# Kernel optimization log

Hardware: AMD Instinct MI355X
Metric: run time of the kernel (lower is better)

The kernel has to match this reference:

```python
import jax, jax.numpy as jnp
import numpy as np

BATCH = 32768


def _unpack(packed, n):
    # packed: [rows, ceil(n/8)] ints in [0,256). Extract bits MSB-first per byte.
    bits = (packed[:, :, None] >> jnp.arange(7, -1, -1, dtype=packed.dtype)) & 1
    return bits.reshape(packed.shape[0], -1)[:, :n]  # [rows, n] of {0,1}


def setup_inputs() -> dict:
    key = jax.random.key(0)
    k0, k1, k2, k3, k4 = jax.random.split(key, 5)
    return {
        "x": jax.random.normal(k0, (BATCH, 784), dtype=jnp.float32),
        "w1_packed": jax.random.randint(k1, (256, 98), 0, 256, dtype=jnp.int32),
        "m1_packed": jax.random.randint(k2, (256, 98), 0, 256, dtype=jnp.int32),
        "alpha1": jnp.float32(1.0),
        "w2_packed": jax.random.randint(k3, (10, 32), 0, 256, dtype=jnp.int32),
        "m2_packed": jax.random.randint(k4, (10, 32), 0, 256, dtype=jnp.int32),
        "alpha2": jnp.float32(1.0),
    }


def reference(x, w1_packed, m1_packed, alpha1, w2_packed, m2_packed, alpha2):
    # Layer 1: binary {-1,+1} weights * {0,1} mask * alpha
    w1 = (2 * _unpack(w1_packed, 784) - 1).astype(jnp.float32)
    w1 = w1 * _unpack(m1_packed, 784).astype(jnp.float32) * alpha1  # [256, 784]
    h = jax.nn.relu(jnp.einsum('bi,oi->bo', x, w1))  # [B, 256]
    # Layer 2
    w2 = (2 * _unpack(w2_packed, 256) - 1).astype(jnp.float32)
    w2 = w2 * _unpack(m2_packed, 256).astype(jnp.float32) * alpha2  # [10, 256]
    return jnp.einsum('bh,oh->bo', h, w2)  # [B, 10]
```

## Files before the change

kernel.cpp:

```cpp
#include <hip/hip_runtime.h>
#include <hip/hip_bf16.h>

typedef __bf16 bf16x8 __attribute__((ext_vector_type(8)));
typedef float floatx4 __attribute__((ext_vector_type(4)));

#define GLB_AS __attribute__((address_space(1)))
#define LDS_AS __attribute__((address_space(3)))

__device__ __forceinline__ void async_cp16(const void* g, void* l) {
  __builtin_amdgcn_global_load_lds((GLB_AS void*)g, (LDS_AS void*)l, 16, 0, 0);
}

__device__ __forceinline__ unsigned short f2bf(float f) {
  __bf16 b = (__bf16)f;
  return __builtin_bit_cast(unsigned short, b);
}

__global__ void decode_w1_kernel(const int* __restrict__ w1p,
                                 const int* __restrict__ m1p,
                                 unsigned short* __restrict__ w1d) {
  int t = blockIdx.x * 256 + threadIdx.x;
  if (t >= 256 * 100) return;
  int r = t / 100;
  int j = t - r * 100;
  unsigned short vals[8];
#pragma unroll
  for (int k = 0; k < 8; ++k) vals[k] = 0;
  if (j < 98) {
    unsigned int v = (unsigned int)w1p[r * 98 + j];
    unsigned int m = (unsigned int)m1p[r * 98 + j];
#pragma unroll
    for (int k = 0; k < 8; ++k) {
      unsigned int bit = (v >> (7 - k)) & 1u;
      unsigned int mk  = (m >> (7 - k)) & 1u;
      vals[k] = (unsigned short)(mk ? (bit ? 0x3F80u : 0xBF80u) : 0u);
    }
  }
  uint4 pack;
  pack.x = (unsigned)vals[0] | ((unsigned)vals[1] << 16);
  pack.y = (unsigned)vals[2] | ((unsigned)vals[3] << 16);
  pack.z = (unsigned)vals[4] | ((unsigned)vals[5] << 16);
  pack.w = (unsigned)vals[6] | ((unsigned)vals[7] << 16);
  *reinterpret_cast<uint4*>(w1d + t * 8) = pack;
}

#define BM 64
#define BK 32
#define NCH 25
#define W1LD 800
#define HS_LD 264

#define OFF_WS0 0
#define OFF_WS1 8192
#define OFF_XS0 16384
#define OFF_XS1 18432
#define OFF_HS  0
#define OFF_W2  16896

__global__ __launch_bounds__(256, 2) void fused_kernel(
    const float* __restrict__ x,
    const unsigned short* __restrict__ w1d,
    const int* __restrict__ w2p,
    const int* __restrict__ m2p,
    const float* __restrict__ a1p,
    const float* __restrict__ a2p,
    float* __restrict__ out) {
  __shared__ unsigned short smem[64 * 264 + 16 * 256];

  const int tid  = threadIdx.x;
  const int wave = tid >> 6;
  const int lane = tid & 63;
  const int l15  = lane & 15;
  const int quad = lane >> 4;
  const int row0 = blockIdx.x * BM;

  floatx4 acc[4][4];
#pragma unroll
  for (int i = 0; i < 4; ++i)
#pragma unroll
    for (int j = 0; j < 4; ++j) acc[i][j] = (floatx4){0.f, 0.f, 0.f, 0.f};

  auto stage_w = [&](int kc, int offW) {
#pragma unroll
    for (int it = 0; it < 4; ++it) {
      int seg = it * 256 + tid;
      int r = seg >> 2, c = seg & 3;
      async_cp16(w1d + r * W1LD + kc * BK + c * 8, &smem[offW + seg * 8]);
    }
  };
  auto load_x = [&](int kc, float4* xv) {
#pragma unroll
    for (int it = 0; it < 2; ++it) {
      int seg = it * 256 + tid;
      int r = seg >> 3, c4 = seg & 7;
      int col = kc * BK + c4 * 4;
      if (col < 784) {
        xv[it] = *reinterpret_cast<const float4*>(
            x + (size_t)(row0 + r) * 784 + col);
      } else {
        xv[it] = (float4){0.f, 0.f, 0.f, 0.f};
      }
    }
  };
  auto cvt_write = [&](int offX, const float4* xv) {
#pragma unroll
    for (int it = 0; it < 2; ++it) {
      int seg = it * 256 + tid;
      int r = seg >> 3, c4 = seg & 7;
      ushort4 b;
      b.x = f2bf(xv[it].x); b.y = f2bf(xv[it].y);
      b.z = f2bf(xv[it].z); b.w = f2bf(xv[it].w);
      *reinterpret_cast<ushort4*>(&smem[offX + r * BK + c4 * 4]) = b;
    }
  };
  auto compute = [&](int offW, int offX) {
    bf16x8 af[4], bfr[4];
#pragma unroll
    for (int mi = 0; mi < 4; ++mi)
      af[mi] = *reinterpret_cast<const bf16x8*>(
          &smem[offX + (mi * 16 + l15) * BK + quad * 8]);
#pragma unroll
    for (int nj = 0; nj < 4; ++nj)
      bfr[nj] = *reinterpret_cast<const bf16x8*>(
          &smem[offW + (wave * 64 + nj * 16 + l15) * BK + quad * 8]);
#pragma unroll
    for (int mi = 0; mi < 4; ++mi)
#pragma unroll
      for (int nj = 0; nj < 4; ++nj)
        acc[mi][nj] = __builtin_amdgcn_mfma_f32_16x16x32_bf16(
            af[mi], bfr[nj], acc[mi][nj], 0, 0, 0);
  };

  {
    float4 xv[2];
    load_x(0, xv);
    stage_w(0, OFF_WS0);
    cvt_write(OFF_XS0, xv);
  }
  __syncthreads();

#pragma unroll 2
  for (int kc = 0; kc < NCH - 1; ++kc) {
    const int p = kc & 1;
    float4 xn[2];
    load_x(kc + 1, xn);
    stage_w(kc + 1, p ? OFF_WS0 : OFF_WS1);
    compute(p ? OFF_WS1 : OFF_WS0,
            p ? OFF_XS1 : OFF_XS0);
    cvt_write(p ? OFF_XS0 : OFF_XS1, xn);
    __syncthreads();
  }
  compute(OFF_WS0, OFF_XS0);
  __syncthreads();

  const float a1 = a1p[0];
  const float a2 = a2p[0];
#pragma unroll
  for (int mi = 0; mi < 4; ++mi) {
#pragma unroll
    for (int nj = 0; nj < 4; ++nj) {
      int col   = wave * 64 + nj * 16 + l15;
      int rbase = mi * 16 + quad * 4;
#pragma unroll
      for (int r = 0; r < 4; ++r) {
        float h = fmaxf(a1 * acc[mi][nj][r], 0.f);
        smem[OFF_HS + (rbase + r) * HS_LD + col] = f2bf(h);
      }
    }
  }
#pragma unroll
  for (int it = 0; it < 2; ++it) {
    int idx = it * 256 + tid;
    if (idx < 320) {
      int r = idx >> 5, j = idx & 31;
      unsigned int v = (unsigned int)w2p[r * 32 + j];
      unsigned int m = (unsigned int)m2p[r * 32 + j];
#pragma unroll
      for (int k = 0; k < 8; ++k) {
        unsigned int bit = (v >> (7 - k)) & 1u;
        unsigned int mk  = (m >> (7 - k)) & 1u;
        smem[OFF_W2 + r * 256 + j * 8 + k] =
            (unsigned short)(mk ? (bit ? 0x3F80u : 0xBF80u) : 0u);
      }
    }
  }
#pragma unroll
  for (int r = 10; r < 16; ++r) smem[OFF_W2 + r * 256 + tid] = 0;
  __syncthreads();

  floatx4 o2 = (floatx4){0.f, 0.f, 0.f, 0.f};
#pragma unroll
  for (int ks = 0; ks < 8; ++ks) {
    bf16x8 ha = *reinterpret_cast<const bf16x8*>(
        &smem[OFF_HS + (wave * 16 + l15) * HS_LD + ks * 32 + quad * 8]);
    bf16x8 wb = *reinterpret_cast<const bf16x8*>(
        &smem[OFF_W2 + l15 * 256 + ks * 32 + quad * 8]);
    o2 = __builtin_amdgcn_mfma_f32_16x16x32_bf16(ha, wb, o2, 0, 0, 0);
  }
  if (l15 < 10) {
#pragma unroll
    for (int r = 0; r < 4; ++r) {
      int gr = row0 + wave * 16 + quad * 4 + r;
      out[(size_t)gr * 10 + l15] = a2 * o2[r];
    }
  }
}

extern "C" void kernel_launch(void* const* d_in, const int* in_sizes, int n_in,
                              void* d_out, int out_size, void* d_ws, size_t ws_size,
                              hipStream_t stream) {
  const float* x   = (const float*)d_in[0];
  const int*   w1p = (const int*)d_in[1];
  const int*   m1p = (const int*)d_in[2];
  const float* a1  = (const float*)d_in[3];
  const int*   w2p = (const int*)d_in[4];
  const int*   m2p = (const int*)d_in[5];
  const float* a2  = (const float*)d_in[6];
  unsigned short* w1d = (unsigned short*)d_ws;
  float* out = (float*)d_out;

  decode_w1_kernel<<<100, 256, 0, stream>>>(w1p, m1p, w1d);
  fused_kernel<<<512, 256, 0, stream>>>(x, w1d, w2p, m2p, a1, a2, out);
}
```

Measured before the change: 181.2 us.

## Use 512-thread blocks with k-group-major LDS layouts and pre-tiled W1

```diff
diff --git a/kernel.cpp b/kernel.cpp
--- a/kernel.cpp
+++ b/kernel.cpp
@@ -18,11 +18,10 @@
 
 __global__ void decode_w1_kernel(const int* __restrict__ w1p,
                                  const int* __restrict__ m1p,
-                                 unsigned short* __restrict__ w1d) {
+                                 unsigned short* __restrict__ w1t) {
   int t = blockIdx.x * 256 + threadIdx.x;
-  if (t >= 256 * 100) return;
-  int r = t / 100;
-  int j = t - r * 100;
+  int r = t & 255;
+  int j = t >> 8;
   unsigned short vals[8];
 #pragma unroll
   for (int k = 0; k < 8; ++k) vals[k] = 0;
@@ -41,14 +40,14 @@
   pack.y = (unsigned)vals[2] | ((unsigned)vals[3] << 16);
   pack.z = (unsigned)vals[4] | ((unsigned)vals[5] << 16);
   pack.w = (unsigned)vals[6] | ((unsigned)vals[7] << 16);
-  *reinterpret_cast<uint4*>(w1d + t * 8) = pack;
+  *reinterpret_cast<uint4*>(w1t + t * 8) = pack;
 }
 
 #define BM 64
 #define BK 32
 #define NCH 25
-#define W1LD 800
 #define HS_LD 264
+#define W2_LD 264
 
 #define OFF_WS0 0
 #define OFF_WS1 8192
@@ -57,15 +56,15 @@
 #define OFF_HS  0
 #define OFF_W2  16896
 
-__global__ __launch_bounds__(256, 2) void fused_kernel(
+__global__ __launch_bounds__(512, 4) void fused_kernel(
     const float* __restrict__ x,
-    const unsigned short* __restrict__ w1d,
+    const unsigned short* __restrict__ w1t,
     const int* __restrict__ w2p,
     const int* __restrict__ m2p,
     const float* __restrict__ a1p,
     const float* __restrict__ a2p,
     float* __restrict__ out) {
-  __shared__ unsigned short smem[64 * 264 + 16 * 256];
+  __shared__ unsigned short smem[64 * HS_LD + 16 * W2_LD];
 
   const int tid  = threadIdx.x;
   const int wave = tid >> 6;
@@ -74,65 +73,59 @@
   const int quad = lane >> 4;
   const int row0 = blockIdx.x * BM;
 
-  floatx4 acc[4][4];
+  floatx4 acc[4][2];
 #pragma unroll
   for (int i = 0; i < 4; ++i)
 #pragma unroll
-    for (int j = 0; j < 4; ++j) acc[i][j] = (floatx4){0.f, 0.f, 0.f, 0.f};
+    for (int j = 0; j < 2; ++j) acc[i][j] = (floatx4){0.f, 0.f, 0.f, 0.f};
+
+  const int xr  = tid >> 3;
+  const int xc4 = tid & 7;
+  const int xq  = xc4 >> 1;
+  const int xh  = xc4 & 1;
+  const float* xbase = x + (size_t)(row0 + xr) * 784 + xc4 * 4;
+  const int xs_off = (xq * 64 + xr) * 8 + xh * 4;
 
   auto stage_w = [&](int kc, int offW) {
 #pragma unroll
-    for (int it = 0; it < 4; ++it) {
-      int seg = it * 256 + tid;
-      int r = seg >> 2, c = seg & 3;
-      async_cp16(w1d + r * W1LD + kc * BK + c * 8, &smem[offW + seg * 8]);
-    }
-  };
-  auto load_x = [&](int kc, float4* xv) {
-#pragma unroll
     for (int it = 0; it < 2; ++it) {
-      int seg = it * 256 + tid;
-      int r = seg >> 3, c4 = seg & 7;
-      int col = kc * BK + c4 * 4;
-      if (col < 784) {
-        xv[it] = *reinterpret_cast<const float4*>(
-            x + (size_t)(row0 + r) * 784 + col);
-      } else {
-        xv[it] = (float4){0.f, 0.f, 0.f, 0.f};
-      }
-    }
-  };
-  auto cvt_write = [&](int offX, const float4* xv) {
-#pragma unroll
-    for (int it = 0; it < 2; ++it) {
-      int seg = it * 256 + tid;
-      int r = seg >> 3, c4 = seg & 7;
-      ushort4 b;
-      b.x = f2bf(xv[it].x); b.y = f2bf(xv[it].y);
-      b.z = f2bf(xv[it].z); b.w = f2bf(xv[it].w);
-      *reinterpret_cast<ushort4*>(&smem[offX + r * BK + c4 * 4]) = b;
-    }
+      int seg = it * 512 + tid;
+      async_cp16(w1t + (size_t)kc * 8192 + seg * 8, &smem[offW + seg * 8]);
+    }
+  };
+  auto load_x = [&](int kc, float4& xv) {
+    int col = kc * BK + xc4 * 4;
+    if (col < 784) {
+      xv = *reinterpret_cast<const float4*>(xbase + kc * BK);
+    } else {
+      xv = (float4){0.f, 0.f, 0.f, 0.f};
+    }
+  };
+  auto cvt_write = [&](int offX, const float4& xv) {
+    ushort4 b;
+    b.x = f2bf(xv.x); b.y = f2bf(xv.y); b.z = f2bf(xv.z); b.w = f2bf(xv.w);
+    *reinterpret_cast<ushort4*>(&smem[offX + xs_off]) = b;
   };
   auto compute = [&](int offW, int offX) {
-    bf16x8 af[4], bfr[4];
+    bf16x8 af[4], bfr[2];
 #pragma unroll
     for (int mi = 0; mi < 4; ++mi)
       af[mi] = *reinterpret_cast<const bf16x8*>(
-          &smem[offX + (mi * 16 + l15) * BK + quad * 8]);
-#pragma unroll
-    for (int nj = 0; nj < 4; ++nj)
+          &smem[offX + (quad * 64 + mi * 16 + l15) * 8]);
+#pragma unroll
+    for (int nj = 0; nj < 2; ++nj)
       bfr[nj] = *reinterpret_cast<const bf16x8*>(
-          &smem[offW + (wave * 64 + nj * 16 + l15) * BK + quad * 8]);
+          &smem[offW + (quad * 256 + wave * 32 + nj * 16 + l15) * 8]);
 #pragma unroll
     for (int mi = 0; mi < 4; ++mi)
 #pragma unroll
-      for (int nj = 0; nj < 4; ++nj)
+      for (int nj = 0; nj < 2; ++nj)
         acc[mi][nj] = __builtin_amdgcn_mfma_f32_16x16x32_bf16(
             af[mi], bfr[nj], acc[mi][nj], 0, 0, 0);
   };
 
   {
-    float4 xv[2];
+    float4 xv;
     load_x(0, xv);
     stage_w(0, OFF_WS0);
     cvt_write(OFF_XS0, xv);
@@ -142,7 +135,7 @@
 #pragma unroll 2
   for (int kc = 0; kc < NCH - 1; ++kc) {
     const int p = kc & 1;
-    float4 xn[2];
+    float4 xn;
     load_x(kc + 1, xn);
     stage_w(kc + 1, p ? OFF_WS0 : OFF_WS1);
     compute(p ? OFF_WS1 : OFF_WS0,
@@ -158,8 +151,8 @@
 #pragma unroll
   for (int mi = 0; mi < 4; ++mi) {
 #pragma unroll
-    for (int nj = 0; nj < 4; ++nj) {
-      int col   = wave * 64 + nj * 16 + l15;
+    for (int nj = 0; nj < 2; ++nj) {
+      int col   = wave * 32 + nj * 16 + l15;
       int rbase = mi * 16 + quad * 4;
 #pragma unroll
       for (int r = 0; r < 4; ++r) {
@@ -168,40 +161,40 @@
       }
     }
   }
-#pragma unroll
-  for (int it = 0; it < 2; ++it) {
-    int idx = it * 256 + tid;
-    if (idx < 320) {
-      int r = idx >> 5, j = idx & 31;
-      unsigned int v = (unsigned int)w2p[r * 32 + j];
-      unsigned int m = (unsigned int)m2p[r * 32 + j];
-#pragma unroll
-      for (int k = 0; k < 8; ++k) {
-        unsigned int bit = (v >> (7 - k)) & 1u;
-        unsigned int mk  = (m >> (7 - k)) & 1u;
-        smem[OFF_W2 + r * 256 + j * 8 + k] =
-            (unsigned short)(mk ? (bit ? 0x3F80u : 0xBF80u) : 0u);
+  if (tid < 320) {
+    int r = tid >> 5, j = tid & 31;
+    unsigned int v = (unsigned int)w2p[r * 32 + j];
+    unsigned int m = (unsigned int)m2p[r * 32 + j];
+#pragma unroll
+    for (int k = 0; k < 8; ++k) {
+      unsigned int bit = (v >> (7 - k)) & 1u;
+      unsigned int mk  = (m >> (7 - k)) & 1u;
+      smem[OFF_W2 + r * W2_LD + j * 8 + k] =
+          (unsigned short)(mk ? (bit ? 0x3F80u : 0xBF80u) : 0u);
+    }
+  }
+  for (int idx = tid; idx < 6 * 256; idx += 512) {
+    int r = 10 + (idx >> 8), c = idx & 255;
+    smem[OFF_W2 + r * W2_LD + c] = 0;
+  }
+  __syncthreads();
+
+  if (wave < 4) {
+    floatx4 o2 = (floatx4){0.f, 0.f, 0.f, 0.f};
+#pragma unroll
+    for (int ks = 0; ks < 8; ++ks) {
+      bf16x8 ha = *reinterpret_cast<const bf16x8*>(
+          &smem[OFF_HS + (wave * 16 + l15) * HS_LD + ks * 32 + quad * 8]);
+      bf16x8 wb = *reinterpret_cast<const bf16x8*>(
+          &smem[OFF_W2 + l15 * W2_LD + ks * 32 + quad * 8]);
+      o2 = __builtin_amdgcn_mfma_f32_16x16x32_bf16(ha, wb, o2, 0, 0, 0);
+    }
+    if (l15 < 10) {
+#pragma unroll
+      for (int r = 0; r < 4; ++r) {
+        int gr = row0 + wave * 16 + quad * 4 + r;
+        out[(size_t)gr * 10 + l15] = a2 * o2[r];
       }
-    }
-  }
-#pragma unroll
-  for (int r = 10; r < 16; ++r) smem[OFF_W2 + r * 256 + tid] = 0;
-  __syncthreads();
-
-  floatx4 o2 = (floatx4){0.f, 0.f, 0.f, 0.f};
-#pragma unroll
-  for (int ks = 0; ks < 8; ++ks) {
-    bf16x8 ha = *reinterpret_cast<const bf16x8*>(
-        &smem[OFF_HS + (wave * 16 + l15) * HS_LD + ks * 32 + quad * 8]);
-    bf16x8 wb = *reinterpret_cast<const bf16x8*>(
-        &smem[OFF_W2 + l15 * 256 + ks * 32 + quad * 8]);
-    o2 = __builtin_amdgcn_mfma_f32_16x16x32_bf16(ha, wb, o2, 0, 0, 0);
-  }
-  if (l15 < 10) {
-#pragma unroll
-    for (int r = 0; r < 4; ++r) {
-      int gr = row0 + wave * 16 + quad * 4 + r;
-      out[(size_t)gr * 10 + l15] = a2 * o2[r];
     }
   }
 }
@@ -216,9 +209,9 @@
   const int*   w2p = (const int*)d_in[4];
   const int*   m2p = (const int*)d_in[5];
   const float* a2  = (const float*)d_in[6];
-  unsigned short* w1d = (unsigned short*)d_ws;
+  unsigned short* w1t = (unsigned short*)d_ws;
   float* out = (float*)d_out;
 
-  decode_w1_kernel<<<100, 256, 0, stream>>>(w1p, m1p, w1d);
-  fused_kernel<<<512, 256, 0, stream>>>(x, w1d, w2p, m2p, a1, a2, out);
-}
+  decode_w1_kernel<<<100, 256, 0, stream>>>(w1p, m1p, w1t);
+  fused_kernel<<<512, 512, 0, stream>>>(x, w1t, w2p, m2p, a1, a2, out);
+}
```

New measurement: 171.7 us. -5.2%, faster.
